# Performance work log

Hardware: AMD Instinct MI355X
Metric: run time of the kernel (lower is better)

## Reference

```python
import jax, jax.numpy as jnp
import numpy as np

H = 64   # hidden_size
L = 64   # num_layers
T = 2    # timesteps
B = 16384
F = 1    # feature_size
O = 1    # output_size


def _uniform(key, shape, bound):
    return jax.random.uniform(key, shape, jnp.float32, -bound, bound)


def setup_inputs() -> dict:
    key = jax.random.key(0)
    ks = jax.random.split(key, 12)
    bound = 1.0 / np.sqrt(H)  # torch default init for GRU/Linear
    return {
        "x": jax.random.normal(ks[0], (B, T, F), jnp.float32),
        "W_ih0": _uniform(ks[1], (3 * H, F), bound),
        "W_hh0": _uniform(ks[2], (3 * H, H), bound),
        "b_ih0": _uniform(ks[3], (3 * H,), bound),
        "b_hh0": _uniform(ks[4], (3 * H,), bound),
        "W_ih": _uniform(ks[5], (L - 1, 3 * H, H), bound),
        "W_hh": _uniform(ks[6], (L - 1, 3 * H, H), bound),
        "b_ih": _uniform(ks[7], (L - 1, 3 * H), bound),
        "b_hh": _uniform(ks[8], (L - 1, 3 * H), bound),
        "Wf": _uniform(ks[9], (O, H), bound),
        "bf": _uniform(ks[10], (O,), bound),
    }


def _gru_layer(seq, Wi, Wh, bi, bh):
    # seq: [T, B, in] -> [T, B, H].  PyTorch gate order: r, z, n.
    gi = jnp.einsum("tbf,gf->tbg", seq, Wi) + bi  # precompute input GEMM for all steps
    h0 = jnp.zeros((seq.shape[1], H), seq.dtype)

    def step(h, gi_t):
        gh = h @ Wh.T + bh
        i_r, i_z, i_n = jnp.split(gi_t, 3, axis=-1)
        h_r, h_z, h_n = jnp.split(gh, 3, axis=-1)
        r = jax.nn.sigmoid(i_r + h_r)
        z = jax.nn.sigmoid(i_z + h_z)
        n = jnp.tanh(i_n + r * h_n)
        h_new = (1.0 - z) * n + z * h
        return h_new, h_new

    _, out = jax.lax.scan(step, h0, gi)
    return out


def reference(x, W_ih0, W_hh0, b_ih0, b_hh0, W_ih, W_hh, b_ih, b_hh, Wf, bf):
    seq = jnp.transpose(x, (1, 0, 2))  # [T, B, F] (batch_first -> time-major)
    seq = _gru_layer(seq, W_ih0, W_hh0, b_ih0, b_hh0)  # layer 0 (input size F)

    def layer_body(s, p):
        Wi, Wh, bi, bh = p
        return _gru_layer(s, Wi, Wh, bi, bh), None

    seq, _ = jax.lax.scan(layer_body, seq, (W_ih, W_hh, b_ih, b_hh))  # layers 1..L-1

    out_flat = jnp.transpose(seq, (1, 0, 2)).reshape(-1, H)  # [B*T, H], batch-major flatten
    y = (out_flat @ Wf.T + bf).reshape(T, B, -1)  # faithful to original reshape
    return y[-1]  # [B, O]
```

## Files before the change

kernel.cpp:

```cpp
#include <hip/hip_runtime.h>


typedef __attribute__((ext_vector_type(8))) short short8;
typedef __attribute__((ext_vector_type(4))) float f32x4;

#define MFMA16(a, b, c) __builtin_amdgcn_mfma_f32_16x16x32_bf16((a), (b), (c), 0, 0, 0)

namespace {

constexpr int kH    = 64;
constexpr int kL    = 64;
constexpr int kB    = 16384;
constexpr int kRPB  = 32;
constexpr int kGrid = (kB / 2) / kRPB;
constexpr int kBlk  = 512;
constexpr int kXP   = 72;
constexpr int kI1P  = 194;
constexpr int kH0P  = 66;

constexpr size_t nWi      = (size_t)63 * 192 * 64;
constexpr size_t nWh      = (size_t)64 * 192 * 64;
constexpr size_t oWiHi    = 0;
constexpr size_t oWiLo    = oWiHi + nWi;
constexpr size_t oWhHi    = oWiLo + nWi;
constexpr size_t oWhLo    = oWhHi + nWh;
constexpr size_t oShortEnd= oWhLo + nWh;
constexpr size_t nB1      = (size_t)64 * 192;
constexpr size_t oBi      = 0;
constexpr size_t oBh      = nB1;

__device__ __forceinline__ unsigned short rne_bf16(float f) {
    unsigned u = __float_as_uint(f);
    return (unsigned short)((u + 0x7FFFu + ((u >> 16) & 1u)) >> 16);
}
__device__ __forceinline__ float bf2f(unsigned short s) {
    return __uint_as_float(((unsigned)s) << 16);
}
__device__ __forceinline__ float sigm(float v) {
    float e = __expf(-v);
    return __builtin_amdgcn_rcpf(1.0f + e);
}
__device__ __forceinline__ float tanh_fast(float v) {
    float e = __expf(-2.0f * v);
    return (1.0f - e) * __builtin_amdgcn_rcpf(1.0f + e);
}

}

extern "C" __global__ void gru_prep(const float* __restrict__ Whh0,
                                    const float* __restrict__ bih0,
                                    const float* __restrict__ bhh0,
                                    const float* __restrict__ WihL,
                                    const float* __restrict__ WhhL,
                                    const float* __restrict__ bihL,
                                    const float* __restrict__ bhhL,
                                    short* __restrict__ wsS,
                                    float* __restrict__ wsF)
{
    int idx = (int)blockIdx.x * 256 + (int)threadIdx.x;
    const int nWiT = 63 * 192 * 64;
    const int nWhT = 64 * 192 * 64;
    const int nBT  = 64 * 192;

    if (idx < nWiT) {
        const int li  = idx / (192 * 64);
        const int rem = idx % (192 * 64);
        const int n = rem / 64, k = rem % 64;
        const int jq = n / 48, g = (n % 48) / 16, jc = n % 16;
        const int row = g * 64 + jq * 16 + jc;
        const float w = WihL[(size_t)li * 192 * 64 + row * 64 + k];
        const unsigned short hi = rne_bf16(w);
        wsS[oWiHi + idx] = (short)hi;
        wsS[oWiLo + idx] = (short)rne_bf16(w - bf2f(hi));
        return;
    }
    idx -= nWiT;
    if (idx < nWhT) {
        const int li  = idx / (192 * 64);
        const int rem = idx % (192 * 64);
        const int n = rem / 64, k = rem % 64;
        const int jq = n / 48, g = (n % 48) / 16, jc = n % 16;
        const int row = g * 64 + jq * 16 + jc;
        const float w = (li == 0) ? Whh0[row * 64 + k]
                                  : WhhL[(size_t)(li - 1) * 192 * 64 + row * 64 + k];
        const unsigned short hi = rne_bf16(w);
        wsS[oWhHi + idx] = (short)hi;
        wsS[oWhLo + idx] = (short)rne_bf16(w - bf2f(hi));
        return;
    }
    idx -= nWhT;
    if (idx < nBT) {
        const int li = idx / 192, n = idx % 192;
        const int jq = n / 48, g = (n % 48) / 16, jc = n % 16;
        const int row = g * 64 + jq * 16 + jc;
        wsF[oBi + idx] = (li == 0) ? bih0[row] : bihL[(size_t)(li - 1) * 192 + row];
        return;
    }
    idx -= nBT;
    if (idx < nBT) {
        const int li = idx / 192, n = idx % 192;
        const int jq = n / 48, g = (n % 48) / 16, jc = n % 16;
        const int row = g * 64 + jq * 16 + jc;
        wsF[oBh + idx] = (li == 0) ? bhh0[row] : bhhL[(size_t)(li - 1) * 192 + row];
        return;
    }
}

extern "C" __global__ __launch_bounds__(kBlk, 2)
void gru_mfma(const float* __restrict__ x,
              const float* __restrict__ Wih0,
              const float* __restrict__ Wf,
              const float* __restrict__ bfp,
              const short* __restrict__ wsS,
              const float* __restrict__ wsF,
              float* __restrict__ out)
{
    __shared__ short Xhi[2][2 * kRPB][kXP];
    __shared__ short Xlo[2][2 * kRPB][kXP];
    __shared__ float H0f[kRPB][kH0P];
    __shared__ float I1[kRPB][kI1P];

    const int tid  = (int)threadIdx.x;
    const int lane = tid & 63;
    const int l15  = lane & 15;
    const int l4   = lane >> 4;
    const int jw   = __builtin_amdgcn_readfirstlane(tid >> 6);
    const int jg   = jw & 3;
    const int mg   = jw >> 2;
    const int rowbase = kB / 2 + (int)blockIdx.x * kRPB;

    const int n0    = jg * 48 + l15;
    const int jcol  = jg * 16 + l15;
    const int koff  = l4 * 8;
    const int wfbase = n0 * 64 + koff;

    short8 wiHi[3][2], wiLo[3][2];

    #pragma unroll 1
    for (int l = 0; l < kL; ++l) {
        const int rb = l & 1, wb = rb ^ 1;

        f32x4 acc[2][3];
        #pragma unroll
        for (int mt = 0; mt < 2; ++mt)
            #pragma unroll
            for (int g = 0; g < 3; ++g)
                acc[mt][g] = f32x4{0.f, 0.f, 0.f, 0.f};

        if (l == 0) {
            float wv[3];
            #pragma unroll
            for (int g = 0; g < 3; ++g) wv[g] = Wih0[g * 64 + jg * 16 + l15];
            #pragma unroll
            for (int mt = 0; mt < 2; ++mt)
                #pragma unroll
                for (int r = 0; r < 4; ++r) {
                    const int trow = mg * 32 + mt * 16 + l4 * 4 + r;
                    const float xv = x[(rowbase + (trow & 31)) * 2 + (trow >> 5)];
                    #pragma unroll
                    for (int g = 0; g < 3; ++g) acc[mt][g][r] = wv[g] * xv;
                }
        } else {
            short8 ahi[2][2], alo[2][2];
            #pragma unroll
            for (int mt = 0; mt < 2; ++mt)
                #pragma unroll
                for (int ks = 0; ks < 2; ++ks) {
                    const int arow = mg * 32 + mt * 16 + l15;
                    ahi[mt][ks] = *reinterpret_cast<const short8*>(&Xhi[rb][arow][ks * 32 + koff]);
                    alo[mt][ks] = *reinterpret_cast<const short8*>(&Xlo[rb][arow][ks * 32 + koff]);
                }
            #pragma unroll
            for (int mt = 0; mt < 2; ++mt)
                #pragma unroll
                for (int g = 0; g < 3; ++g)
                    #pragma unroll
                    for (int ks = 0; ks < 2; ++ks) {
                        acc[mt][g] = MFMA16(ahi[mt][ks], wiHi[g][ks], acc[mt][g]);
                        acc[mt][g] = MFMA16(ahi[mt][ks], wiLo[g][ks], acc[mt][g]);
                        acc[mt][g] = MFMA16(alo[mt][ks], wiHi[g][ks], acc[mt][g]);
                    }
        }

        short8 whHi[3][2], whLo[3][2];
        {
            const short* bh_ = wsS + oWhHi + (size_t)l * 192 * 64;
            const short* bl_ = wsS + oWhLo + (size_t)l * 192 * 64;
            #pragma unroll
            for (int g = 0; g < 3; ++g)
                #pragma unroll
                for (int ks = 0; ks < 2; ++ks) {
                    const int off = wfbase + g * 1024 + ks * 32;
                    whHi[g][ks] = *reinterpret_cast<const short8*>(bh_ + off);
                    whLo[g][ks] = *reinterpret_cast<const short8*>(bl_ + off);
                }
        }

        const float* biL = wsF + oBi + (size_t)l * 192;
        const float* bhL = wsF + oBh + (size_t)l * 192;
        float bi_[3], bh_[3];
        #pragma unroll
        for (int g = 0; g < 3; ++g) { bi_[g] = biL[n0 + g * 16]; bh_[g] = bhL[n0 + g * 16]; }

        if (mg == 0) {
            #pragma unroll
            for (int mt = 0; mt < 2; ++mt)
                #pragma unroll
                for (int r = 0; r < 4; ++r) {
                    const int trow = mt * 16 + l4 * 4 + r;
                    const float r0 = sigm(acc[mt][0][r] + bi_[0] + bh_[0]);
                    const float z0 = sigm(acc[mt][1][r] + bi_[1] + bh_[1]);
                    const float n0v = tanh_fast(acc[mt][2][r] + bi_[2] + r0 * bh_[2]);
                    const float h0 = (1.0f - z0) * n0v;
                    H0f[trow][jcol] = h0;
                    const unsigned short h = rne_bf16(h0);
                    Xhi[wb][trow][jcol] = (short)h;
                    Xlo[wb][trow][jcol] = (short)rne_bf16(h0 - bf2f(h));
                }
        } else {
            #pragma unroll
            for (int mt = 0; mt < 2; ++mt)
                #pragma unroll
                for (int r = 0; r < 4; ++r) {
                    const int trow = mt * 16 + l4 * 4 + r;
                    I1[trow][n0]      = acc[mt][0][r] + bi_[0];
                    I1[trow][n0 + 16] = acc[mt][1][r] + bi_[1];
                    I1[trow][n0 + 32] = acc[mt][2][r] + bi_[2];
                }
        }
        __syncthreads();

        f32x4 acc2[3];
        #pragma unroll
        for (int g = 0; g < 3; ++g) acc2[g] = f32x4{0.f, 0.f, 0.f, 0.f};
        {
            short8 hhi[2], hlo[2];
            #pragma unroll
            for (int ks = 0; ks < 2; ++ks) {
                const int hrow = mg * 16 + l15;
                hhi[ks] = *reinterpret_cast<const short8*>(&Xhi[wb][hrow][ks * 32 + koff]);
                hlo[ks] = *reinterpret_cast<const short8*>(&Xlo[wb][hrow][ks * 32 + koff]);
            }
            #pragma unroll
            for (int g = 0; g < 3; ++g)
                #pragma unroll
                for (int ks = 0; ks < 2; ++ks) {
                    acc2[g] = MFMA16(hhi[ks], whHi[g][ks], acc2[g]);
                    acc2[g] = MFMA16(hhi[ks], whLo[g][ks], acc2[g]);
                    acc2[g] = MFMA16(hlo[ks], whHi[g][ks], acc2[g]);
                }
        }

        if (l < kL - 1) {
            const short* bh_ = wsS + oWiHi + (size_t)l * 192 * 64;
            const short* bl_ = wsS + oWiLo + (size_t)l * 192 * 64;
            #pragma unroll
            for (int g = 0; g < 3; ++g)
                #pragma unroll
                for (int ks = 0; ks < 2; ++ks) {
                    const int off = wfbase + g * 1024 + ks * 32;
                    wiHi[g][ks] = *reinterpret_cast<const short8*>(bh_ + off);
                    wiLo[g][ks] = *reinterpret_cast<const short8*>(bl_ + off);
                }
        }

        #pragma unroll
        for (int r = 0; r < 4; ++r) {
            const int row = mg * 16 + l4 * 4 + r;
            const float hr = acc2[0][r] + bh_[0];
            const float hz = acc2[1][r] + bh_[1];
            const float hn = acc2[2][r] + bh_[2];
            const float r1 = sigm(I1[row][n0] + hr);
            const float z1 = sigm(I1[row][n0 + 16] + hz);
            const float n1v = tanh_fast(I1[row][n0 + 32] + r1 * hn);
            const float h1 = (1.0f - z1) * n1v + z1 * H0f[row][jcol];
            const unsigned short h = rne_bf16(h1);
            Xhi[wb][32 + row][jcol] = (short)h;
            Xlo[wb][32 + row][jcol] = (short)rne_bf16(h1 - bf2f(h));
        }
        __syncthreads();
    }

    if (jw == 0) {
        float a = 0.0f;
        #pragma unroll
        for (int k = 0; k < kH; ++k) {
            const float hv = bf2f((unsigned short)Xhi[0][lane][k]) +
                             bf2f((unsigned short)Xlo[0][lane][k]);
            a = fmaf(Wf[k], hv, a);
        }
        out[2 * ((int)blockIdx.x * kRPB + (lane & 31)) + (lane >> 5)] = a + bfp[0];
    }
}

extern "C" void kernel_launch(void* const* d_in, const int* in_sizes, int n_in,
                              void* d_out, int out_size, void* d_ws, size_t ws_size,
                              hipStream_t stream) {
    const float* x    = (const float*)d_in[0];
    const float* Wih0 = (const float*)d_in[1];
    const float* Whh0 = (const float*)d_in[2];
    const float* bih0 = (const float*)d_in[3];
    const float* bhh0 = (const float*)d_in[4];
    const float* WihL = (const float*)d_in[5];
    const float* WhhL = (const float*)d_in[6];
    const float* bihL = (const float*)d_in[7];
    const float* bhhL = (const float*)d_in[8];
    const float* Wf   = (const float*)d_in[9];
    const float* bfp  = (const float*)d_in[10];

    short* wsS = (short*)d_ws;
    float* wsF = (float*)((char*)d_ws + oShortEnd * sizeof(short));

    const int prepThreads = 1585152;
    gru_prep<<<dim3(prepThreads / 256), dim3(256), 0, stream>>>(
        Whh0, bih0, bhh0, WihL, WhhL, bihL, bhhL, wsS, wsF);

    gru_mfma<<<dim3(kGrid), dim3(kBlk), 0, stream>>>(
        x, Wih0, Wf, bfp, wsS, wsF, (float*)d_out);
}
```

Before: 448.7 us.

## Wavefront-pipeline GRU layers across timesteps with split warp roles and vectorized prep

Restructures the GRU kernel so half of the warps compute layer l+1 at timestep 0 while the other half compute layer l at timestep 1, in a diagonal wavefront. This removes one of the two barriers per layer. Rows per block are halved and the launch bound raised to allow more blocks per CU. Weights are now streamed from global memory each layer instead of held in registers. The prep kernel is vectorized to process four weights per thread. The trade-offs are more weight reloads across more blocks and per-layer global loads on the critical path.

Result: slower. 653.0 us (+45.5%).

```diff
diff --git a/kernel.cpp b/kernel.cpp
--- a/kernel.cpp
+++ b/kernel.cpp
@@ -2,6 +2,7 @@
 
 
 typedef __attribute__((ext_vector_type(8))) short short8;
+typedef __attribute__((ext_vector_type(4))) short short4v;
 typedef __attribute__((ext_vector_type(4))) float f32x4;
 
 #define MFMA16(a, b, c) __builtin_amdgcn_mfma_f32_16x16x32_bf16((a), (b), (c), 0, 0, 0)
@@ -11,23 +12,22 @@
 constexpr int kH    = 64;
 constexpr int kL    = 64;
 constexpr int kB    = 16384;
-constexpr int kRPB  = 32;
+constexpr int kRPB  = 16;
 constexpr int kGrid = (kB / 2) / kRPB;
 constexpr int kBlk  = 512;
 constexpr int kXP   = 72;
-constexpr int kI1P  = 194;
-constexpr int kH0P  = 66;
-
-constexpr size_t nWi      = (size_t)63 * 192 * 64;
-constexpr size_t nWh      = (size_t)64 * 192 * 64;
-constexpr size_t oWiHi    = 0;
-constexpr size_t oWiLo    = oWiHi + nWi;
-constexpr size_t oWhHi    = oWiLo + nWi;
-constexpr size_t oWhLo    = oWhHi + nWh;
-constexpr size_t oShortEnd= oWhLo + nWh;
-constexpr size_t nB1      = (size_t)64 * 192;
-constexpr size_t oBi      = 0;
-constexpr size_t oBh      = nB1;
+constexpr int kH0P  = 68;
+
+constexpr size_t nWi       = (size_t)63 * 192 * 64;
+constexpr size_t nWh       = (size_t)64 * 192 * 64;
+constexpr size_t oWiHi     = 0;
+constexpr size_t oWiLo     = oWiHi + nWi;
+constexpr size_t oWhHi     = oWiLo + nWi;
+constexpr size_t oWhLo     = oWhHi + nWh;
+constexpr size_t oShortEnd = oWhLo + nWh;
+constexpr size_t nB1       = (size_t)64 * 192;
+constexpr size_t oBi       = 0;
+constexpr size_t oBh       = nB1;
 
 __device__ __forceinline__ unsigned short rne_bf16(float f) {
     unsigned u = __float_as_uint(f);
@@ -58,37 +58,53 @@
                                     float* __restrict__ wsF)
 {
     int idx = (int)blockIdx.x * 256 + (int)threadIdx.x;
-    const int nWiT = 63 * 192 * 64;
-    const int nWhT = 64 * 192 * 64;
+    const int nWi4 = 63 * 192 * 16;
+    const int nWh4 = 64 * 192 * 16;
     const int nBT  = 64 * 192;
 
-    if (idx < nWiT) {
-        const int li  = idx / (192 * 64);
-        const int rem = idx % (192 * 64);
-        const int n = rem / 64, k = rem % 64;
+    if (idx < nWi4) {
+        const int li  = idx / (192 * 16);
+        const int rem = idx % (192 * 16);
+        const int n = rem >> 4, k4 = rem & 15;
         const int jq = n / 48, g = (n % 48) / 16, jc = n % 16;
         const int row = g * 64 + jq * 16 + jc;
-        const float w = WihL[(size_t)li * 192 * 64 + row * 64 + k];
-        const unsigned short hi = rne_bf16(w);
-        wsS[oWiHi + idx] = (short)hi;
-        wsS[oWiLo + idx] = (short)rne_bf16(w - bf2f(hi));
+        const f32x4 w = *reinterpret_cast<const f32x4*>(
+            WihL + (size_t)li * 12288 + row * 64 + k4 * 4);
+        short4v hi, lo;
+        #pragma unroll
+        for (int e = 0; e < 4; ++e) {
+            const unsigned short h = rne_bf16(w[e]);
+            hi[e] = (short)h;
+            lo[e] = (short)rne_bf16(w[e] - bf2f(h));
+        }
+        const size_t off = (size_t)li * 12288 + n * 64 + k4 * 4;
+        *reinterpret_cast<short4v*>(wsS + oWiHi + off) = hi;
+        *reinterpret_cast<short4v*>(wsS + oWiLo + off) = lo;
         return;
     }
-    idx -= nWiT;
-    if (idx < nWhT) {
-        const int li  = idx / (192 * 64);
-        const int rem = idx % (192 * 64);
-        const int n = rem / 64, k = rem % 64;
+    idx -= nWi4;
+    if (idx < nWh4) {
+        const int li  = idx / (192 * 16);
+        const int rem = idx % (192 * 16);
+        const int n = rem >> 4, k4 = rem & 15;
         const int jq = n / 48, g = (n % 48) / 16, jc = n % 16;
         const int row = g * 64 + jq * 16 + jc;
-        const float w = (li == 0) ? Whh0[row * 64 + k]
-                                  : WhhL[(size_t)(li - 1) * 192 * 64 + row * 64 + k];
-        const unsigned short hi = rne_bf16(w);
-        wsS[oWhHi + idx] = (short)hi;
-        wsS[oWhLo + idx] = (short)rne_bf16(w - bf2f(hi));
+        const float* src = (li == 0) ? (Whh0 + row * 64 + k4 * 4)
+                                     : (WhhL + (size_t)(li - 1) * 12288 + row * 64 + k4 * 4);
+        const f32x4 w = *reinterpret_cast<const f32x4*>(src);
+        short4v hi, lo;
+        #pragma unroll
+        for (int e = 0; e < 4; ++e) {
+            const unsigned short h = rne_bf16(w[e]);
+            hi[e] = (short)h;
+            lo[e] = (short)rne_bf16(w[e] - bf2f(h));
+        }
+        const size_t off = (size_t)li * 12288 + n * 64 + k4 * 4;
+        *reinterpret_cast<short4v*>(wsS + oWhHi + off) = hi;
+        *reinterpret_cast<short4v*>(wsS + oWhLo + off) = lo;
         return;
     }
-    idx -= nWhT;
+    idx -= nWh4;
     if (idx < nBT) {
         const int li = idx / 192, n = idx % 192;
         const int jq = n / 48, g = (n % 48) / 16, jc = n % 16;
@@ -106,7 +122,7 @@
     }
 }
 
-extern "C" __global__ __launch_bounds__(kBlk, 2)
+extern "C" __global__ __launch_bounds__(kBlk, 4)
 void gru_mfma(const float* __restrict__ x,
               const float* __restrict__ Wih0,
               const float* __restrict__ Wf,
@@ -115,181 +131,213 @@
               const float* __restrict__ wsF,
               float* __restrict__ out)
 {
-    __shared__ short Xhi[2][2 * kRPB][kXP];
-    __shared__ short Xlo[2][2 * kRPB][kXP];
-    __shared__ float H0f[kRPB][kH0P];
-    __shared__ float I1[kRPB][kI1P];
+    __shared__ __align__(16) short X0hi[2][kRPB][kXP];
+    __shared__ __align__(16) short X0lo[2][kRPB][kXP];
+    __shared__ __align__(16) short X1hi[2][kRPB][kXP];
+    __shared__ __align__(16) short X1lo[2][kRPB][kXP];
+    __shared__ __align__(16) float H0f[2][kRPB][kH0P];
 
     const int tid  = (int)threadIdx.x;
     const int lane = tid & 63;
     const int l15  = lane & 15;
     const int l4   = lane >> 4;
     const int jw   = __builtin_amdgcn_readfirstlane(tid >> 6);
-    const int jg   = jw & 3;
-    const int mg   = jw >> 2;
-    const int rowbase = kB / 2 + (int)blockIdx.x * kRPB;
-
-    const int n0    = jg * 48 + l15;
-    const int jcol  = jg * 16 + l15;
-    const int koff  = l4 * 8;
-    const int wfbase = n0 * 64 + koff;
-
-    short8 wiHi[3][2], wiLo[3][2];
+    const int jq   = jw & 3;
+    const int wt   = jw >> 2;
+    const int grow = kB / 2 + (int)blockIdx.x * kRPB + l15;
+
+    const float xv0 = x[grow * 2 + 0];
+    const float xv1 = x[grow * 2 + 1];
+
+    const int col4  = jq * 16 + l4 * 4;
+    const int wbase = (jq * 48 + l15) * 64 + l4 * 8;
+    const int xoff  = l4 * 8;
+
+    if (wt == 1) {
+        const float* biL = wsF + oBi + jq * 48 + l4 * 4;
+        const float* bhL = wsF + oBh + jq * 48 + l4 * 4;
+        const f32x4 w0 = *reinterpret_cast<const f32x4*>(Wih0 + 0 * 64 + col4);
+        const f32x4 w1 = *reinterpret_cast<const f32x4*>(Wih0 + 1 * 64 + col4);
+        const f32x4 w2 = *reinterpret_cast<const f32x4*>(Wih0 + 2 * 64 + col4);
+        const f32x4 bi0 = *reinterpret_cast<const f32x4*>(biL);
+        const f32x4 bi1 = *reinterpret_cast<const f32x4*>(biL + 16);
+        const f32x4 bi2 = *reinterpret_cast<const f32x4*>(biL + 32);
+        const f32x4 bh0 = *reinterpret_cast<const f32x4*>(bhL);
+        const f32x4 bh1 = *reinterpret_cast<const f32x4*>(bhL + 16);
+        const f32x4 bh2 = *reinterpret_cast<const f32x4*>(bhL + 32);
+        short4v ohi, olo; f32x4 fh;
+        #pragma unroll
+        for (int r = 0; r < 4; ++r) {
+            const float rr = sigm(w0[r] * xv0 + bi0[r] + bh0[r]);
+            const float zz = sigm(w1[r] * xv0 + bi1[r] + bh1[r]);
+            const float nn = tanh_fast(w2[r] * xv0 + bi2[r] + rr * bh2[r]);
+            const float h0 = (1.0f - zz) * nn;
+            fh[r] = h0;
+            const unsigned short h = rne_bf16(h0);
+            ohi[r] = (short)h;
+            olo[r] = (short)rne_bf16(h0 - bf2f(h));
+        }
+        *reinterpret_cast<f32x4*>(&H0f[0][l15][col4])   = fh;
+        *reinterpret_cast<short4v*>(&X0hi[0][l15][col4]) = ohi;
+        *reinterpret_cast<short4v*>(&X0lo[0][l15][col4]) = olo;
+    }
+    __syncthreads();
 
     #pragma unroll 1
     for (int l = 0; l < kL; ++l) {
         const int rb = l & 1, wb = rb ^ 1;
 
-        f32x4 acc[2][3];
-        #pragma unroll
-        for (int mt = 0; mt < 2; ++mt)
-            #pragma unroll
-            for (int g = 0; g < 3; ++g)
-                acc[mt][g] = f32x4{0.f, 0.f, 0.f, 0.f};
-
-        if (l == 0) {
-            float wv[3];
-            #pragma unroll
-            for (int g = 0; g < 3; ++g) wv[g] = Wih0[g * 64 + jg * 16 + l15];
-            #pragma unroll
-            for (int mt = 0; mt < 2; ++mt)
+        if (wt == 0) {
+            f32x4 ai[3], ah[3];
+            #pragma unroll
+            for (int g = 0; g < 3; ++g) {
+                ai[g] = f32x4{0.f, 0.f, 0.f, 0.f};
+                ah[g] = f32x4{0.f, 0.f, 0.f, 0.f};
+            }
+
+            if (l == 0) {
+                const f32x4 w0 = *reinterpret_cast<const f32x4*>(Wih0 + 0 * 64 + col4);
+                const f32x4 w1 = *reinterpret_cast<const f32x4*>(Wih0 + 1 * 64 + col4);
+                const f32x4 w2 = *reinterpret_cast<const f32x4*>(Wih0 + 2 * 64 + col4);
                 #pragma unroll
                 for (int r = 0; r < 4; ++r) {
-                    const int trow = mg * 32 + mt * 16 + l4 * 4 + r;
-                    const float xv = x[(rowbase + (trow & 31)) * 2 + (trow >> 5)];
-                    #pragma unroll
-                    for (int g = 0; g < 3; ++g) acc[mt][g][r] = wv[g] * xv;
+                    ai[0][r] = w0[r] * xv1;
+                    ai[1][r] = w1[r] * xv1;
+                    ai[2][r] = w2[r] * xv1;
                 }
-        } else {
-            short8 ahi[2][2], alo[2][2];
-            #pragma unroll
-            for (int mt = 0; mt < 2; ++mt)
+            } else {
+                short8 xh[2], xl[2];
                 #pragma unroll
                 for (int ks = 0; ks < 2; ++ks) {
-                    const int arow = mg * 32 + mt * 16 + l15;
-                    ahi[mt][ks] = *reinterpret_cast<const short8*>(&Xhi[rb][arow][ks * 32 + koff]);
-                    alo[mt][ks] = *reinterpret_cast<const short8*>(&Xlo[rb][arow][ks * 32 + koff]);
+                    xh[ks] = *reinterpret_cast<const short8*>(&X1hi[rb][l15][ks * 32 + xoff]);
+                    xl[ks] = *reinterpret_cast<const short8*>(&X1lo[rb][l15][ks * 32 + xoff]);
                 }
-            #pragma unroll
-            for (int mt = 0; mt < 2; ++mt)
+                const short* WiH = wsS + oWiHi + (size_t)(l - 1) * 12288;
+                const short* WiL = wsS + oWiLo + (size_t)(l - 1) * 12288;
                 #pragma unroll
                 for (int g = 0; g < 3; ++g)
                     #pragma unroll
                     for (int ks = 0; ks < 2; ++ks) {
-                        acc[mt][g] = MFMA16(ahi[mt][ks], wiHi[g][ks], acc[mt][g]);
-                        acc[mt][g] = MFMA16(ahi[mt][ks], wiLo[g][ks], acc[mt][g]);
-                        acc[mt][g] = MFMA16(alo[mt][ks], wiHi[g][ks], acc[mt][g]);
+                        const short8 wh_ = *reinterpret_cast<const short8*>(WiH + wbase + g * 1024 + ks * 32);
+                        const short8 wl_ = *reinterpret_cast<const short8*>(WiL + wbase + g * 1024 + ks * 32);
+                        ai[g] = MFMA16(wh_, xh[ks], ai[g]);
+                        ai[g] = MFMA16(wl_, xh[ks], ai[g]);
+                        ai[g] = MFMA16(wh_, xl[ks], ai[g]);
                     }
-        }
-
-        short8 whHi[3][2], whLo[3][2];
-        {
-            const short* bh_ = wsS + oWhHi + (size_t)l * 192 * 64;
-            const short* bl_ = wsS + oWhLo + (size_t)l * 192 * 64;
+            }
+            {
+                short8 hh[2], hl[2];
+                #pragma unroll
+                for (int ks = 0; ks < 2; ++ks) {
+                    hh[ks] = *reinterpret_cast<const short8*>(&X0hi[rb][l15][ks * 32 + xoff]);
+                    hl[ks] = *reinterpret_cast<const short8*>(&X0lo[rb][l15][ks * 32 + xoff]);
+                }
+                const short* WhH = wsS + oWhHi + (size_t)l * 12288;
+                const short* WhL = wsS + oWhLo + (size_t)l * 12288;
+                #pragma unroll
+                for (int g = 0; g < 3; ++g)
+                    #pragma unroll
+                    for (int ks = 0; ks < 2; ++ks) {
+                        const short8 wh_ = *reinterpret_cast<const short8*>(WhH + wbase + g * 1024 + ks * 32);
+                        const short8 wl_ = *reinterpret_cast<const short8*>(WhL + wbase + g * 1024 + ks * 32);
+                        ah[g] = MFMA16(wh_, hh[ks], ah[g]);
+                        ah[g] = MFMA16(wl_, hh[ks], ah[g]);
+                        ah[g] = MFMA16(wh_, hl[ks], ah[g]);
+                    }
+            }
+            const float* biL = wsF + oBi + (size_t)l * 192 + jq * 48 + l4 * 4;
+            const float* bhL = wsF + oBh + (size_t)l * 192 + jq * 48 + l4 * 4;
+            const f32x4 bi0 = *reinterpret_cast<const f32x4*>(biL);
+            const f32x4 bi1 = *reinterpret_cast<const f32x4*>(biL + 16);
+            const f32x4 bi2 = *reinterpret_cast<const f32x4*>(biL + 32);
+            const f32x4 bh0 = *reinterpret_cast<const f32x4*>(bhL);
+            const f32x4 bh1 = *reinterpret_cast<const f32x4*>(bhL + 16);
+            const f32x4 bh2 = *reinterpret_cast<const f32x4*>(bhL + 32);
+            const f32x4 h0v = *reinterpret_cast<const f32x4*>(&H0f[rb][l15][col4]);
+            short4v ohi, olo;
+            #pragma unroll
+            for (int r = 0; r < 4; ++r) {
+                const float rr = sigm(ai[0][r] + bi0[r] + ah[0][r] + bh0[r]);
+                const float zz = sigm(ai[1][r] + bi1[r] + ah[1][r] + bh1[r]);
+                const float nn = tanh_fast(ai[2][r] + bi2[r] + rr * (ah[2][r] + bh2[r]));
+                const float h1 = (1.0f - zz) * nn + zz * h0v[r];
+                const unsigned short h = rne_bf16(h1);
+                ohi[r] = (short)h;
+                olo[r] = (short)rne_bf16(h1 - bf2f(h));
+            }
+            *reinterpret_cast<short4v*>(&X1hi[wb][l15][col4]) = ohi;
+            *reinterpret_cast<short4v*>(&X1lo[wb][l15][col4]) = olo;
+        } else if (l < kL - 1) {
+            f32x4 a0[3];
+            #pragma unroll
+            for (int g = 0; g < 3; ++g) a0[g] = f32x4{0.f, 0.f, 0.f, 0.f};
+            short8 hh[2], hl[2];
+            #pragma unroll
+            for (int ks = 0; ks < 2; ++ks) {
+                hh[ks] = *reinterpret_cast<const short8*>(&X0hi[rb][l15][ks * 32 + xoff]);
+                hl[ks] = *reinterpret_cast<const short8*>(&X0lo[rb][l15][ks * 32 + xoff]);
+            }
+            const short* WiH = wsS + oWiHi + (size_t)l * 12288;
+            const short* WiL = wsS + oWiLo + (size_t)l * 12288;
             #pragma unroll
             for (int g = 0; g < 3; ++g)
                 #pragma unroll
                 for (int ks = 0; ks < 2; ++ks) {
-                    const int off = wfbase + g * 1024 + ks * 32;
-                    whHi[g][ks] = *reinterpret_cast<const short8*>(bh_ + off);
-                    whLo[g][ks] = *reinterpret_cast<const short8*>(bl_ + off);
+                    const short8 wh_ = *reinterpret_cast<const short8*>(WiH + wbase + g * 1024 + ks * 32);
+                    const short8 wl_ = *reinterpret_cast<const short8*>(WiL + wbase + g * 1024 + ks * 32);
+                    a0[g] = MFMA16(wh_, hh[ks], a0[g]);
+                    a0[g] = MFMA16(wl_, hh[ks], a0[g]);
+                    a0[g] = MFMA16(wh_, hl[ks], a0[g]);
                 }
-        }
-
-        const float* biL = wsF + oBi + (size_t)l * 192;
-        const float* bhL = wsF + oBh + (size_t)l * 192;
-        float bi_[3], bh_[3];
-        #pragma unroll
-        for (int g = 0; g < 3; ++g) { bi_[g] = biL[n0 + g * 16]; bh_[g] = bhL[n0 + g * 16]; }
-
-        if (mg == 0) {
-            #pragma unroll
-            for (int mt = 0; mt < 2; ++mt)
-                #pragma unroll
-                for (int r = 0; r < 4; ++r) {
-                    const int trow = mt * 16 + l4 * 4 + r;
-                    const float r0 = sigm(acc[mt][0][r] + bi_[0] + bh_[0]);
-                    const float z0 = sigm(acc[mt][1][r] + bi_[1] + bh_[1]);
-                    const float n0v = tanh_fast(acc[mt][2][r] + bi_[2] + r0 * bh_[2]);
-                    const float h0 = (1.0f - z0) * n0v;
-                    H0f[trow][jcol] = h0;
-                    const unsigned short h = rne_bf16(h0);
-                    Xhi[wb][trow][jcol] = (short)h;
-                    Xlo[wb][trow][jcol] = (short)rne_bf16(h0 - bf2f(h));
-                }
+            const float* biL = wsF + oBi + (size_t)(l + 1) * 192 + jq * 48 + l4 * 4;
+            const float* bhL = wsF + oBh + (size_t)(l + 1) * 192 + jq * 48 + l4 * 4;
+            const f32x4 bi0 = *reinterpret_cast<const f32x4*>(biL);
+            const f32x4 bi1 = *reinterpret_cast<const f32x4*>(biL + 16);
+            const f32x4 bi2 = *reinterpret_cast<const f32x4*>(biL + 32);
+            const f32x4 bh0 = *reinterpret_cast<const f32x4*>(bhL);
+            const f32x4 bh1 = *reinterpret_cast<const f32x4*>(bhL + 16);
+            const f32x4 bh2 = *reinterpret_cast<const f32x4*>(bhL + 32);
+            short4v ohi, olo; f32x4 fh;
+            #pragma unroll
+            for (int r = 0; r < 4; ++r) {
+                const float rr = sigm(a0[0][r] + bi0[r] + bh0[r]);
+                const float zz = sigm(a0[1][r] + bi1[r] + bh1[r]);
+                const float nn = tanh_fast(a0[2][r] + bi2[r] + rr * bh2[r]);
+                const float h0 = (1.0f - zz) * nn;
+                fh[r] = h0;
+                const unsigned short h = rne_bf16(h0);
+                ohi[r] = (short)h;
+                olo[r] = (short)rne_bf16(h0 - bf2f(h));
+            }
+            *reinterpret_cast<f32x4*>(&H0f[wb][l15][col4])   = fh;
+            *reinterpret_cast<short4v*>(&X0hi[wb][l15][col4]) = ohi;
+            *reinterpret_cast<short4v*>(&X0lo[wb][l15][col4]) = olo;
+        }
+        __syncthreads();
+    }
+
+    if (tid < 32) {
+        const int row = tid & 15, t = tid >> 4;
+        float a = 0.0f;
+        if (t == 0) {
+            #pragma unroll
+            for (int c = 0; c < 16; ++c) {
+                const f32x4 hv = *reinterpret_cast<const f32x4*>(&H0f[1][row][c * 4]);
+                #pragma unroll
+                for (int e = 0; e < 4; ++e) a = fmaf(Wf[c * 4 + e], hv[e], a);
+            }
         } else {
             #pragma unroll
-            for (int mt = 0; mt < 2; ++mt)
-                #pragma unroll
-                for (int r = 0; r < 4; ++r) {
-                    const int trow = mt * 16 + l4 * 4 + r;
-                    I1[trow][n0]      = acc[mt][0][r] + bi_[0];
-                    I1[trow][n0 + 16] = acc[mt][1][r] + bi_[1];
-                    I1[trow][n0 + 32] = acc[mt][2][r] + bi_[2];
-                }
-        }
-        __syncthreads();
-
-        f32x4 acc2[3];
-        #pragma unroll
-        for (int g = 0; g < 3; ++g) acc2[g] = f32x4{0.f, 0.f, 0.f, 0.f};
-        {
-            short8 hhi[2], hlo[2];
-            #pragma unroll
-            for (int ks = 0; ks < 2; ++ks) {
-                const int hrow = mg * 16 + l15;
-                hhi[ks] = *reinterpret_cast<const short8*>(&Xhi[wb][hrow][ks * 32 + koff]);
-                hlo[ks] = *reinterpret_cast<const short8*>(&Xlo[wb][hrow][ks * 32 + koff]);
-            }
-            #pragma unroll
-            for (int g = 0; g < 3; ++g)
-                #pragma unroll
-                for (int ks = 0; ks < 2; ++ks) {
-                    acc2[g] = MFMA16(hhi[ks], whHi[g][ks], acc2[g]);
-                    acc2[g] = MFMA16(hhi[ks], whLo[g][ks], acc2[g]);
-                    acc2[g] = MFMA16(hlo[ks], whHi[g][ks], acc2[g]);
-                }
-        }
-
-        if (l < kL - 1) {
-            const short* bh_ = wsS + oWiHi + (size_t)l * 192 * 64;
-            const short* bl_ = wsS + oWiLo + (size_t)l * 192 * 64;
-            #pragma unroll
-            for (int g = 0; g < 3; ++g)
-                #pragma unroll
-                for (int ks = 0; ks < 2; ++ks) {
-                    const int off = wfbase + g * 1024 + ks * 32;
-                    wiHi[g][ks] = *reinterpret_cast<const short8*>(bh_ + off);
-                    wiLo[g][ks] = *reinterpret_cast<const short8*>(bl_ + off);
-                }
-        }
-
-        #pragma unroll
-        for (int r = 0; r < 4; ++r) {
-            const int row = mg * 16 + l4 * 4 + r;
-            const float hr = acc2[0][r] + bh_[0];
-            const float hz = acc2[1][r] + bh_[1];
-            const float hn = acc2[2][r] + bh_[2];
-            const float r1 = sigm(I1[row][n0] + hr);
-            const float z1 = sigm(I1[row][n0 + 16] + hz);
-            const float n1v = tanh_fast(I1[row][n0 + 32] + r1 * hn);
-            const float h1 = (1.0f - z1) * n1v + z1 * H0f[row][jcol];
-            const unsigned short h = rne_bf16(h1);
-            Xhi[wb][32 + row][jcol] = (short)h;
-            Xlo[wb][32 + row][jcol] = (short)rne_bf16(h1 - bf2f(h));
-        }
-        __syncthreads();
-    }
-
-    if (jw == 0) {
-        float a = 0.0f;
-        #pragma unroll
-        for (int k = 0; k < kH; ++k) {
-            const float hv = bf2f((unsigned short)Xhi[0][lane][k]) +
-                             bf2f((unsigned short)Xlo[0][lane][k]);
-            a = fmaf(Wf[k], hv, a);
-        }
-        out[2 * ((int)blockIdx.x * kRPB + (lane & 31)) + (lane >> 5)] = a + bfp[0];
+            for (int c = 0; c < 8; ++c) {
+                const short8 hv = *reinterpret_cast<const short8*>(&X1hi[0][row][c * 8]);
+                const short8 lv = *reinterpret_cast<const short8*>(&X1lo[0][row][c * 8]);
+                #pragma unroll
+                for (int e = 0; e < 8; ++e)
+                    a = fmaf(Wf[c * 8 + e],
+                             bf2f((unsigned short)hv[e]) + bf2f((unsigned short)lv[e]), a);
+            }
+        }
+        out[2 * ((int)blockIdx.x * kRPB + row) + t] = a + bfp[0];
     }
 }
 
@@ -311,8 +359,7 @@
     short* wsS = (short*)d_ws;
     float* wsF = (float*)((char*)d_ws + oShortEnd * sizeof(short));
 
-    const int prepThreads = 1585152;
-    gru_prep<<<dim3(prepThreads / 256), dim3(256), 0, stream>>>(
+    gru_prep<<<dim3(414720 / 256), dim3(256), 0, stream>>>(
         Whh0, bih0, bhh0, WihL, WhhL, bihL, bhhL, wsS, wsF);
 
     gru_mfma<<<dim3(kGrid), dim3(kBlk), 0, stream>>>(
```
